# Optimization experiments

Measured on AMD Instinct MI355X. Metric: run time of the kernel, lower is better.

The kernel has to match this reference:

```python
import jax, jax.numpy as jnp
import numpy as np

B, C, H, W = 8, 64, 64, 64
CK = C // 8  # query/key channels

def setup_inputs() -> dict:
    key = jax.random.key(0)
    ks = jax.random.split(key, 8)
    x = jax.random.normal(ks[0], (B, C, H, W), dtype=jnp.float32)
    # Conv1d with kernel size 1 == per-position linear map; store weights as [out, in].
    # (Spectral norm only rescales the weight matrix; with given weights the forward
    #  math is an ordinary 1x1 conv.)
    Wq = jax.random.normal(ks[1], (CK, C), dtype=jnp.float32) / np.sqrt(C)
    bq = jnp.zeros((CK,), dtype=jnp.float32)
    Wk = jax.random.normal(ks[2], (CK, C), dtype=jnp.float32) / np.sqrt(C)
    bk = jnp.zeros((CK,), dtype=jnp.float32)
    Wv = jax.random.normal(ks[3], (C, C), dtype=jnp.float32) / np.sqrt(C)
    bv = jnp.zeros((C,), dtype=jnp.float32)
    gamma = jnp.asarray(0.5, dtype=jnp.float32)  # nonzero so attention path matters
    return {"x": x, "Wq": Wq, "bq": bq, "Wk": Wk, "bk": bk, "Wv": Wv, "bv": bv, "gamma": gamma}

def reference(x, Wq, bq, Wk, bk, Wv, bv, gamma):
    b, c, h, w = x.shape
    flat = x.reshape(b, c, h * w)                       # [B, C, L]
    q = jnp.einsum('oc,bcl->blo', Wq, flat) + bq        # [B, L, C/8] (query permuted)
    k = jnp.einsum('oc,bcl->bol', Wk, flat) + bk[None, :, None]   # [B, C/8, L]
    v = jnp.einsum('oc,bcl->bol', Wv, flat) + bv[None, :, None]   # [B, C, L]
    qk = jnp.einsum('blo,bom->blm', q, k)               # [B, L, L]
    attn = jax.nn.softmax(qk, axis=1)                   # softmax over dim 1 (rows)
    out = jnp.einsum('bcl,blm->bcm', v, attn)           # [B, C, L]
    out = out.reshape(b, c, h, w)
    return gamma * out + x
```

## Files before the change

### kernel.cpp

```cpp
#include <hip/hip_runtime.h>
#include <math.h>

#define B_   8
#define C_   64
#define CK_  8
#define L_   4096

typedef __attribute__((ext_vector_type(8))) __bf16 bf16x8;
typedef __attribute__((ext_vector_type(4))) __bf16 bf16x4;
typedef __attribute__((ext_vector_type(4))) float  f32x4;

__global__ __launch_bounds__(256) void qkv_kernel(
    const float* __restrict__ x,
    const float* __restrict__ Wq, const float* __restrict__ bq,
    const float* __restrict__ Wk, const float* __restrict__ bk,
    const float* __restrict__ Wv, const float* __restrict__ bv,
    __bf16* __restrict__ qo, __bf16* __restrict__ ko, __bf16* __restrict__ vpack)
{
    __shared__ float LWq[CK_ * C_];
    __shared__ float LWk[CK_ * C_];
    __shared__ float LWv[C_ * C_];
    __shared__ __bf16 Lqs[64 * 8];
    __shared__ __bf16 Lks[64 * 8];

    const int tid = threadIdx.x;
    if (tid < 128) {
        ((float4*)LWq)[tid] = ((const float4*)Wq)[tid];
        ((float4*)LWk)[tid] = ((const float4*)Wk)[tid];
    }
    #pragma unroll
    for (int j = 0; j < 4; ++j)
        ((float4*)LWv)[tid + j * 256] = ((const float4*)Wv)[tid + j * 256];
    __syncthreads();

    const int b  = blockIdx.x >> 6;
    const int t  = blockIdx.x & 63;
    const int l0 = t << 6;
    const int lg = tid & 15;
    const int g  = tid >> 4;

    float va[4][4];
    float qk[4];
    #pragma unroll
    for (int j = 0; j < 4; ++j) {
        float bb = bv[4 * g + j];
        va[j][0] = bb; va[j][1] = bb; va[j][2] = bb; va[j][3] = bb;
    }
    {
        float bb = (g < 8) ? bq[g] : bk[g - 8];
        qk[0] = bb; qk[1] = bb; qk[2] = bb; qk[3] = bb;
    }
    const float* wqk = (g < 8) ? (LWq + g * C_) : (LWk + (g - 8) * C_);

    const float* xp = x + ((size_t)b * C_) * L_ + l0 + lg * 4;
    #pragma unroll 4
    for (int c4 = 0; c4 < 16; ++c4) {
        float4 xv[4];
        #pragma unroll
        for (int u = 0; u < 4; ++u)
            xv[u] = *(const float4*)(xp + (size_t)(4 * c4 + u) * L_);
        #pragma unroll
        for (int j = 0; j < 4; ++j) {
            float4 wv = ((const float4*)(LWv + (4 * g + j) * C_))[c4];
            float* a = va[j];
            a[0]=fmaf(wv.x,xv[0].x,a[0]); a[1]=fmaf(wv.x,xv[0].y,a[1]); a[2]=fmaf(wv.x,xv[0].z,a[2]); a[3]=fmaf(wv.x,xv[0].w,a[3]);
            a[0]=fmaf(wv.y,xv[1].x,a[0]); a[1]=fmaf(wv.y,xv[1].y,a[1]); a[2]=fmaf(wv.y,xv[1].z,a[2]); a[3]=fmaf(wv.y,xv[1].w,a[3]);
            a[0]=fmaf(wv.z,xv[2].x,a[0]); a[1]=fmaf(wv.z,xv[2].y,a[1]); a[2]=fmaf(wv.z,xv[2].z,a[2]); a[3]=fmaf(wv.z,xv[2].w,a[3]);
            a[0]=fmaf(wv.w,xv[3].x,a[0]); a[1]=fmaf(wv.w,xv[3].y,a[1]); a[2]=fmaf(wv.w,xv[3].z,a[2]); a[3]=fmaf(wv.w,xv[3].w,a[3]);
        }
        {
            float4 wv = ((const float4*)wqk)[c4];
            qk[0]=fmaf(wv.x,xv[0].x,qk[0]); qk[1]=fmaf(wv.x,xv[0].y,qk[1]); qk[2]=fmaf(wv.x,xv[0].z,qk[2]); qk[3]=fmaf(wv.x,xv[0].w,qk[3]);
            qk[0]=fmaf(wv.y,xv[1].x,qk[0]); qk[1]=fmaf(wv.y,xv[1].y,qk[1]); qk[2]=fmaf(wv.y,xv[1].z,qk[2]); qk[3]=fmaf(wv.y,xv[1].w,qk[3]);
            qk[0]=fmaf(wv.z,xv[2].x,qk[0]); qk[1]=fmaf(wv.z,xv[2].y,qk[1]); qk[2]=fmaf(wv.z,xv[2].z,qk[2]); qk[3]=fmaf(wv.z,xv[2].w,qk[3]);
            qk[0]=fmaf(wv.w,xv[3].x,qk[0]); qk[1]=fmaf(wv.w,xv[3].y,qk[1]); qk[2]=fmaf(wv.w,xv[3].z,qk[2]); qk[3]=fmaf(wv.w,xv[3].w,qk[3]);
        }
    }

    {
        __bf16* vt = vpack + ((size_t)b * 64 + t) * 4096;
        const int cb = g >> 2;
        const int sg = lg >> 2;
        const int qd = lg & 3;
        #pragma unroll
        for (int j = 0; j < 4; ++j) {
            bf16x4 vv;
            vv[0]=(__bf16)va[j][0]; vv[1]=(__bf16)va[j][1]; vv[2]=(__bf16)va[j][2]; vv[3]=(__bf16)va[j][3];
            *(bf16x4*)(vt + ((size_t)((cb * 4 + sg) * 64 + qd * 16 + (g & 3) * 4 + j)) * 4) = vv;
        }
    }
    #pragma unroll
    for (int u = 0; u < 4; ++u) {
        if (g < 8) Lqs[(lg * 4 + u) * 8 + g]       = (__bf16)qk[u];
        else       Lks[(lg * 4 + u) * 8 + (g - 8)] = (__bf16)qk[u];
    }
    __syncthreads();
    if (tid < 64) {
        *(bf16x8*)(qo + ((size_t)b * L_ + l0 + tid) * 8) = *(bf16x8*)(Lqs + tid * 8);
        *(bf16x8*)(ko + ((size_t)b * L_ + l0 + tid) * 8) = *(bf16x8*)(Lks + tid * 8);
    }
}

__global__ __launch_bounds__(512, 4) void attn_kernel(
    const __bf16* __restrict__ q, const __bf16* __restrict__ kT,
    const __bf16* __restrict__ VP, const float* __restrict__ x,
    const float* __restrict__ gamma_p, float* __restrict__ out)
{
    __shared__ __bf16 Lv[4][4096];
    __shared__ float  csA[8][16];

    const int tid  = threadIdx.x;
    const int w    = tid >> 6;
    const int lane = tid & 63;
    const int quad = lane >> 4;
    const int l16  = lane & 15;
    const int wh   = w & 3;
    const int lh   = w >> 2;
    const int wg   = blockIdx.x;
    const int b    = wg & 7;
    const int mb   = wg >> 3;
    const int m0   = mb << 6;

    const __bf16* vp = VP + (size_t)b * (64 * 4096);
    const __bf16* qb = q  + (size_t)b * L_ * CK_;

    bf16x8 kf = {};
    if (quad == 0) kf = *(const bf16x8*)(kT + ((size_t)b * L_ + m0 + wh * 16 + l16) * CK_);

    const __bf16* gk[4];
    int ok[4];
    #pragma unroll
    for (int k = 0; k < 4; ++k) {
        const int u = w * 4 + k, tl = u >> 3, seg = u & 7;
        gk[k] = vp + (size_t)((tl & 1) * 32 + (tl >> 1)) * 4096 + seg * 512 + lane * 8;
        ok[k] = tl * 4096 + seg * 512 + lane * 8;
    }

    f32x4 acc[4] = {};
    float csum = 0.f;
    bf16x8 r[4];

    #pragma unroll
    for (int k = 0; k < 4; ++k) r[k] = *(const bf16x8*)gk[k];
    #pragma unroll
    for (int k = 0; k < 4; ++k) *(bf16x8*)(&Lv[0][0] + ok[k]) = r[k];

    for (int i = 0; i < 16; ++i) {
        __syncthreads();

        if (i < 15) {
            #pragma unroll
            for (int k = 0; k < 4; ++k)
                r[k] = *(const bf16x8*)(gk[k] + (size_t)(i + 1) * 8192);
        }

        bf16x8 qA[4], qB[4];
        #pragma unroll
        for (int sg = 0; sg < 4; ++sg) {
            qA[sg] = *(const bf16x8*)(qb + (size_t)((lh * 32 + 2 * i)     * 64 + sg * 16 + l16) * CK_);
            qB[sg] = *(const bf16x8*)(qb + (size_t)((lh * 32 + 2 * i + 1) * 64 + sg * 16 + l16) * CK_);
        }

        bf16x4 pkA[4], pkB[4];
        #pragma unroll
        for (int sg = 0; sg < 4; ++sg) {
            f32x4 sv = __builtin_amdgcn_mfma_f32_16x16x32_bf16(qA[sg], kf, (f32x4){0.f,0.f,0.f,0.f}, 0, 0, 0);
            const float e0 = __expf(sv[0]);
            const float e1 = __expf(sv[1]);
            const float e2 = __expf(sv[2]);
            const float e3 = __expf(sv[3]);
            csum += (e0 + e1) + (e2 + e3);
            pkA[sg][0]=(__bf16)e0; pkA[sg][1]=(__bf16)e1; pkA[sg][2]=(__bf16)e2; pkA[sg][3]=(__bf16)e3;
        }
        #pragma unroll
        for (int sg = 0; sg < 4; ++sg) {
            f32x4 sv = __builtin_amdgcn_mfma_f32_16x16x32_bf16(qB[sg], kf, (f32x4){0.f,0.f,0.f,0.f}, 0, 0, 0);
            const float e0 = __expf(sv[0]);
            const float e1 = __expf(sv[1]);
            const float e2 = __expf(sv[2]);
            const float e3 = __expf(sv[3]);
            csum += (e0 + e1) + (e2 + e3);
            pkB[sg][0]=(__bf16)e0; pkB[sg][1]=(__bf16)e1; pkB[sg][2]=(__bf16)e2; pkB[sg][3]=(__bf16)e3;
        }

        const __bf16* LbA = &Lv[lh][0];
        const __bf16* LbB = &Lv[2 + lh][0];
        #pragma unroll
        for (int sg = 0; sg < 4; ++sg) {
            bf16x8 p8 = __builtin_shufflevector(pkA[sg], pkB[sg], 0, 1, 2, 3, 4, 5, 6, 7);
            #pragma unroll
            for (int cb = 0; cb < 4; ++cb) {
                bf16x4 vfA = *(const bf16x4*)(LbA + ((size_t)((cb * 4 + sg) * 64 + lane)) * 4);
                bf16x4 vfB = *(const bf16x4*)(LbB + ((size_t)((cb * 4 + sg) * 64 + lane)) * 4);
                bf16x8 a8 = __builtin_shufflevector(vfA, vfB, 0, 1, 2, 3, 4, 5, 6, 7);
                acc[cb] = __builtin_amdgcn_mfma_f32_16x16x32_bf16(a8, p8, acc[cb], 0, 0, 0);
            }
        }

        __syncthreads();
        if (i < 15) {
            #pragma unroll
            for (int k = 0; k < 4; ++k)
                *(bf16x8*)(&Lv[0][0] + ok[k]) = r[k];
        }
    }

    float* Sc = (float*)&Lv[0][0];
    if (lh == 1) {
        #pragma unroll
        for (int cb = 0; cb < 4; ++cb)
            #pragma unroll
            for (int r2 = 0; r2 < 4; ++r2)
                Sc[(wh * 64 + cb * 16 + quad * 4 + r2) * 16 + l16] = acc[cb][r2];
    }
    csum += __shfl_xor(csum, 16);
    csum += __shfl_xor(csum, 32);
    if (quad == 0) csA[w][l16] = csum;
    __syncthreads();

    if (lh == 0) {
        const float rinv = gamma_p[0] / (csA[wh][l16] + csA[wh + 4][l16]);
        #pragma unroll
        for (int cb = 0; cb < 4; ++cb) {
            #pragma unroll
            for (int r2 = 0; r2 < 4; ++r2) {
                const int c = cb * 16 + quad * 4 + r2;
                const float vsum = acc[cb][r2] + Sc[(wh * 64 + c) * 16 + l16];
                const size_t idx = ((size_t)(b * 64 + c)) * L_ + m0 + wh * 16 + l16;
                out[idx] = fmaf(rinv, vsum, x[idx]);
            }
        }
    }
}

extern "C" void kernel_launch(void* const* d_in, const int* in_sizes, int n_in,
                              void* d_out, int out_size, void* d_ws, size_t ws_size,
                              hipStream_t stream) {
    const float* x  = (const float*)d_in[0];
    const float* Wq = (const float*)d_in[1];
    const float* bq = (const float*)d_in[2];
    const float* Wk = (const float*)d_in[3];
    const float* bk = (const float*)d_in[4];
    const float* Wv = (const float*)d_in[5];
    const float* bv = (const float*)d_in[6];
    const float* gm = (const float*)d_in[7];
    float* out = (float*)d_out;

    __bf16* ws    = (__bf16*)d_ws;
    __bf16* qo    = ws;
    __bf16* ko    = ws + 262144;
    __bf16* vpack = ws + 524288;

    qkv_kernel<<<dim3(B_ * (L_ / 64)), dim3(256), 0, stream>>>(
        x, Wq, bq, Wk, bk, Wv, bv, qo, ko, vpack);
    attn_kernel<<<dim3(B_ * 64), dim3(512), 0, stream>>>(
        qo, ko, vpack, x, gm, out);
}
```

Measured before the change: 132.3 us.

## Split attention reduction over key halves and stage x tile in LDS

The attention kernel now splits the reduction over the L dimension into two halves, doubling the grid to 1024 workgroups. Each half writes partial bf16 accumulators and column sums to workspace, and a new combine kernel normalises them, applies gamma and adds the residual. The aim is better occupancy and load balance across the CUs. The cost is an extra kernel launch, extra workspace traffic, and bf16 rounding of the partial sums. Separately, qkv_kernel now loads its x tile into shared memory with coalesced row reads, replacing strided global float4 reads per channel.

```diff
diff --git a/kernel.cpp b/kernel.cpp
--- a/kernel.cpp
+++ b/kernel.cpp
@@ -20,10 +20,15 @@
     __shared__ float LWq[CK_ * C_];
     __shared__ float LWk[CK_ * C_];
     __shared__ float LWv[C_ * C_];
+    __shared__ float LX[64][68];
     __shared__ __bf16 Lqs[64 * 8];
     __shared__ __bf16 Lks[64 * 8];
 
     const int tid = threadIdx.x;
+    const int b  = blockIdx.x >> 6;
+    const int t  = blockIdx.x & 63;
+    const int l0 = t << 6;
+
     if (tid < 128) {
         ((float4*)LWq)[tid] = ((const float4*)Wq)[tid];
         ((float4*)LWk)[tid] = ((const float4*)Wk)[tid];
@@ -31,11 +36,15 @@
     #pragma unroll
     for (int j = 0; j < 4; ++j)
         ((float4*)LWv)[tid + j * 256] = ((const float4*)Wv)[tid + j * 256];
+    {
+        const int c = tid >> 2, part = tid & 3;
+        const float* xrow = x + ((size_t)b * C_ + c) * L_ + l0 + part * 16;
+        float4* dst = (float4*)&LX[c][part * 16];
+        #pragma unroll
+        for (int u = 0; u < 4; ++u) dst[u] = ((const float4*)xrow)[u];
+    }
     __syncthreads();
 
-    const int b  = blockIdx.x >> 6;
-    const int t  = blockIdx.x & 63;
-    const int l0 = t << 6;
     const int lg = tid & 15;
     const int g  = tid >> 4;
 
@@ -52,13 +61,12 @@
     }
     const float* wqk = (g < 8) ? (LWq + g * C_) : (LWk + (g - 8) * C_);
 
-    const float* xp = x + ((size_t)b * C_) * L_ + l0 + lg * 4;
     #pragma unroll 4
     for (int c4 = 0; c4 < 16; ++c4) {
         float4 xv[4];
         #pragma unroll
         for (int u = 0; u < 4; ++u)
-            xv[u] = *(const float4*)(xp + (size_t)(4 * c4 + u) * L_);
+            xv[u] = *(const float4*)&LX[4 * c4 + u][lg * 4];
         #pragma unroll
         for (int j = 0; j < 4; ++j) {
             float4 wv = ((const float4*)(LWv + (4 * g + j) * C_))[c4];
@@ -103,8 +111,8 @@
 
 __global__ __launch_bounds__(512, 4) void attn_kernel(
     const __bf16* __restrict__ q, const __bf16* __restrict__ kT,
-    const __bf16* __restrict__ VP, const float* __restrict__ x,
-    const float* __restrict__ gamma_p, float* __restrict__ out)
+    const __bf16* __restrict__ VP,
+    __bf16* __restrict__ pacc, float* __restrict__ pcs)
 {
     __shared__ __bf16 Lv[4][4096];
     __shared__ float  csA[8][16];
@@ -118,7 +126,8 @@
     const int lh   = w >> 2;
     const int wg   = blockIdx.x;
     const int b    = wg & 7;
-    const int mb   = wg >> 3;
+    const int mb   = (wg >> 3) & 63;
+    const int lq   = wg >> 9;
     const int m0   = mb << 6;
 
     const __bf16* vp = VP + (size_t)b * (64 * 4096);
@@ -132,7 +141,7 @@
     #pragma unroll
     for (int k = 0; k < 4; ++k) {
         const int u = w * 4 + k, tl = u >> 3, seg = u & 7;
-        gk[k] = vp + (size_t)((tl & 1) * 32 + (tl >> 1)) * 4096 + seg * 512 + lane * 8;
+        gk[k] = vp + (size_t)(lq * 32 + (tl & 1) * 16 + (tl >> 1)) * 4096 + seg * 512 + lane * 8;
         ok[k] = tl * 4096 + seg * 512 + lane * 8;
     }
 
@@ -145,20 +154,21 @@
     #pragma unroll
     for (int k = 0; k < 4; ++k) *(bf16x8*)(&Lv[0][0] + ok[k]) = r[k];
 
-    for (int i = 0; i < 16; ++i) {
+    for (int i = 0; i < 8; ++i) {
         __syncthreads();
 
-        if (i < 15) {
+        if (i < 7) {
             #pragma unroll
             for (int k = 0; k < 4; ++k)
                 r[k] = *(const bf16x8*)(gk[k] + (size_t)(i + 1) * 8192);
         }
 
+        const int te = lq * 32 + lh * 16 + 2 * i;
         bf16x8 qA[4], qB[4];
         #pragma unroll
         for (int sg = 0; sg < 4; ++sg) {
-            qA[sg] = *(const bf16x8*)(qb + (size_t)((lh * 32 + 2 * i)     * 64 + sg * 16 + l16) * CK_);
-            qB[sg] = *(const bf16x8*)(qb + (size_t)((lh * 32 + 2 * i + 1) * 64 + sg * 16 + l16) * CK_);
+            qA[sg] = *(const bf16x8*)(qb + (size_t)(te * 64 + sg * 16 + l16) * CK_);
+            qB[sg] = *(const bf16x8*)(qb + (size_t)((te + 1) * 64 + sg * 16 + l16) * CK_);
         }
 
         bf16x4 pkA[4], pkB[4];
@@ -198,7 +208,7 @@
         }
 
         __syncthreads();
-        if (i < 15) {
+        if (i < 7) {
             #pragma unroll
             for (int k = 0; k < 4; ++k)
                 *(bf16x8*)(&Lv[0][0] + ok[k]) = r[k];
@@ -218,18 +228,45 @@
     if (quad == 0) csA[w][l16] = csum;
     __syncthreads();
 
+    const size_t pbase = ((size_t)(b * 64 + mb)) * 2 + lq;
     if (lh == 0) {
-        const float rinv = gamma_p[0] / (csA[wh][l16] + csA[wh + 4][l16]);
+        if (quad == 0)
+            pcs[pbase * 64 + wh * 16 + l16] = csA[wh][l16] + csA[wh + 4][l16];
+        __bf16* pa = pacc + pbase * 4096;
         #pragma unroll
         for (int cb = 0; cb < 4; ++cb) {
             #pragma unroll
             for (int r2 = 0; r2 < 4; ++r2) {
                 const int c = cb * 16 + quad * 4 + r2;
                 const float vsum = acc[cb][r2] + Sc[(wh * 64 + c) * 16 + l16];
-                const size_t idx = ((size_t)(b * 64 + c)) * L_ + m0 + wh * 16 + l16;
-                out[idx] = fmaf(rinv, vsum, x[idx]);
+                pa[c * 64 + wh * 16 + l16] = (__bf16)vsum;
             }
         }
+    }
+}
+
+__global__ __launch_bounds__(256) void combine_kernel(
+    const __bf16* __restrict__ pacc, const float* __restrict__ pcs,
+    const float* __restrict__ x, const float* __restrict__ gamma_p,
+    float* __restrict__ out)
+{
+    const int tid = threadIdx.x;
+    const int m  = tid & 63;
+    const int cq = tid >> 6;
+    const int b  = blockIdx.x >> 6;
+    const int mb = blockIdx.x & 63;
+
+    const size_t base = ((size_t)(b * 64 + mb)) * 2;
+    const float csv = pcs[base * 64 + m] + pcs[(base + 1) * 64 + m];
+    const float rinv = gamma_p[0] / csv;
+
+    const __bf16* pa = pacc + base * 4096;
+    #pragma unroll
+    for (int ci = 0; ci < 16; ++ci) {
+        const int c = cq * 16 + ci;
+        const float s = (float)pa[c * 64 + m] + (float)pa[4096 + c * 64 + m];
+        const size_t idx = ((size_t)(b * 64 + c)) * L_ + mb * 64 + m;
+        out[idx] = fmaf(rinv, s, x[idx]);
     }
 }
 
@@ -250,9 +287,13 @@
     __bf16* qo    = ws;
     __bf16* ko    = ws + 262144;
     __bf16* vpack = ws + 524288;
+    __bf16* pacc  = ws + 2621440;
+    float*  pcs   = (float*)(ws + 6815744);
 
     qkv_kernel<<<dim3(B_ * (L_ / 64)), dim3(256), 0, stream>>>(
         x, Wq, bq, Wk, bk, Wv, bv, qo, ko, vpack);
-    attn_kernel<<<dim3(B_ * 64), dim3(512), 0, stream>>>(
-        qo, ko, vpack, x, gm, out);
-}
+    attn_kernel<<<dim3(B_ * 64 * 2), dim3(512), 0, stream>>>(
+        qo, ko, vpack, pacc, pcs);
+    combine_kernel<<<dim3(B_ * 64), dim3(256), 0, stream>>>(
+        pacc, pcs, x, gm, out);
+}
```

Measured after the change: 131.8 us. Within noise of the previous version (-0.4%).
